# Kernel optimization log

Hardware: AMD Instinct MI355X
Metric: run time of the kernel (lower is better)

The kernel has to match this reference:

```python
import jax, jax.numpy as jnp
import numpy as np

N = 100000      # nodes
E = 6400000     # edges (avg degree 64)
S = 8           # FSM states
X = 2 ** S      # neighborhood 'characters' (256)
ITERS = 20      # NeuralFSM.iterations


def setup_inputs() -> dict:
    key = jax.random.key(0)
    k1, k2, k3 = jax.random.split(key, 3)
    # one-hot initial node states [N, S]
    state_idx = jax.random.randint(k1, (N,), 0, S)
    s0 = jax.nn.one_hot(state_idx, S, dtype=jnp.float32)
    # edge list [2, E]
    edge_index = jax.random.randint(k2, (2, E), 0, N, dtype=jnp.int32)
    # FSM transition tensor T[char, state, :] is one-hot over next state -> [X, S, S]
    next_state = jax.random.randint(k3, (X, S), 0, S)
    T = jax.nn.one_hot(next_state, S, dtype=jnp.float32)
    return {"s0": s0, "edge_index": edge_index, "T": T}


def reference(s0, edge_index, T):
    n_nodes, n_states = s0.shape
    src, dst = edge_index[0], edge_index[1]
    powers = (2 ** jnp.arange(n_states)).astype(jnp.int32)  # base-2 encoding of thresholded aggr

    def step(s, _):
        # message = x_j gathered from source nodes, scatter-added at destinations
        msg_sum = jax.ops.segment_sum(s[src], dst, num_segments=n_nodes)  # [N, S]
        # threshold (> 0.5) then clamp to {0,1}
        aggr = (msg_sum > 0.5).astype(jnp.int32)                          # [N, S]
        # multiple-hot -> index into 2^S characters (one-hot folded into a gather)
        idx = aggr @ powers                                               # [N]
        # einsum('x,s,xst->t') with one-hot char == gather T[idx] then contract state
        new_s = jnp.einsum('ns,nst->nt', s, T[idx])                       # [N, S]
        return new_s, None

    s_final, _ = jax.lax.scan(step, s0, None, length=ITERS)
    return s_final
```

## Files before the change

### kernel.cpp

```cpp
#include <hip/hip_runtime.h>
#include <hip/hip_bf16.h>
#include <stdint.h>


#define NN 100000
#define EE 6400000
#define NCHARS 2048
#define ITERS 20

#define NBKT 250
#define NPB 400
#define WPS 12500
#define X4N 3125
#define CEDGE 12800
#define NCHUNK 500
#define CAPB 27648
#define HCAP 13824

#define MEG_TOP     2080
#define CUR_OFF     3328
#define BAR_WORDS   4096

typedef uint32_t u32x4 __attribute__((ext_vector_type(4)));

__device__ inline void mega_barrier(uint32_t* bar, int line, uint32_t epoch) {
    __syncthreads();
    if (threadIdx.x == 0) {
        uint32_t old = atomicAdd(&bar[1664 + line * 16], 1u);
        if (old + 1u == 10u * epoch) {
            uint32_t told = atomicAdd(&bar[MEG_TOP], 1u);
            if (told + 1u == 25u * epoch) {
                for (int r = 0; r < 25; ++r)
                    atomicExch(&bar[2112 + r * 16], epoch);
            }
        }
        while (__hip_atomic_load(&bar[2112 + line * 16], __ATOMIC_RELAXED,
                                 __HIP_MEMORY_SCOPE_AGENT) < epoch)
            __builtin_amdgcn_s_sleep(16);
    }
    __syncthreads();
}

__global__ void __launch_bounds__(512) build_kernel(const int* __restrict__ src,
                                                    const int* __restrict__ dst,
                                                    const float* __restrict__ s0,
                                                    const float* __restrict__ T,
                                                    uint32_t* __restrict__ gPk0,
                                                    uint8_t* __restrict__ nextT,
                                                    uint32_t* __restrict__ csr,
                                                    uint32_t* __restrict__ bar) {
    __shared__ uint32_t stage[CEDGE];
    __shared__ uint32_t cw[8][256];
    __shared__ uint32_t scanb[512];
    __shared__ uint32_t loc[NBKT + 1];
    __shared__ uint32_t segoff[NBKT];
    __shared__ uint8_t  lut[CEDGE];
    int t = threadIdx.x, w = t >> 6;
    int c = blockIdx.x;
    int e0 = c * CEDGE;
    const int4* ps4 = (const int4*)(src + e0);
    const int4* pd4 = (const int4*)(dst + e0);
    uint32_t* cursorG = bar + CUR_OFF;

    if (t < 25) loc[t] = 0;
    __syncthreads();
    if (t < 200) {
        const float* row = s0 + ((size_t)c * 200 + t) * 8;
        int s = 0;
        #pragma unroll
        for (int q = 1; q < 8; ++q) if (row[q] > 0.5f) s = q;
        atomicOr(&loc[t >> 3], (uint32_t)s << ((t & 7) << 2));
    }
    __syncthreads();
    if (t < 25) gPk0[c * 25 + t] = loc[t];
    if (c < 4) {
        const float* row = T + (c * 512 + t) * 8;
        int s = 0;
        #pragma unroll
        for (int q = 1; q < 8; ++q) if (row[q] > 0.5f) s = q;
        nextT[c * 512 + t] = (uint8_t)s;
    }
    __syncthreads();

    for (int i = t; i < 8 * 256; i += 512) ((uint32_t*)cw)[i] = 0;
    __syncthreads();
    for (int i = t; i < CEDGE / 4; i += 512) {
        int4 d = pd4[i];
        atomicAdd(&cw[w][d.x / NPB], 1u);
        atomicAdd(&cw[w][d.y / NPB], 1u);
        atomicAdd(&cw[w][d.z / NPB], 1u);
        atomicAdd(&cw[w][d.w / NPB], 1u);
    }
    __syncthreads();
    uint32_t tot = 0;
    if (t < NBKT) {
        #pragma unroll
        for (int w2 = 0; w2 < 8; ++w2) tot += cw[w2][t];
    }
    scanb[t] = tot;
    __syncthreads();
    for (int off = 1; off < 512; off <<= 1) {
        uint32_t x = (t >= off) ? scanb[t - off] : 0u;
        __syncthreads();
        scanb[t] += x;
        __syncthreads();
    }
    if (t < NBKT) {
        uint32_t excl = scanb[t] - tot;
        loc[t] = excl;
        uint32_t myStart = atomicAdd(&cursorG[t], tot);
        segoff[t] = (uint32_t)t * CAPB + myStart - excl;
        uint32_t acc = excl;
        #pragma unroll
        for (int w2 = 0; w2 < 8; ++w2) {
            uint32_t cv = cw[w2][t];
            cw[w2][t] = acc;
            acc += cv;
        }
    }
    if (t == 0) loc[NBKT] = CEDGE;
    __syncthreads();
    for (int b = t; b < NBKT; b += 512) {
        uint32_t lo = loc[b], hi = loc[b + 1];
        for (uint32_t i = lo; i < hi; ++i) lut[i] = (uint8_t)b;
    }
    for (int i = t; i < CEDGE / 4; i += 512) {
        int4 d = pd4[i];
        int4 s = ps4[i];
        int bb; uint32_t dl, pos;
        bb = d.x / NPB; dl = (uint32_t)(d.x - bb * NPB);
        pos = atomicAdd(&cw[w][bb], 1u); stage[pos] = ((uint32_t)s.x << 9) | dl;
        bb = d.y / NPB; dl = (uint32_t)(d.y - bb * NPB);
        pos = atomicAdd(&cw[w][bb], 1u); stage[pos] = ((uint32_t)s.y << 9) | dl;
        bb = d.z / NPB; dl = (uint32_t)(d.z - bb * NPB);
        pos = atomicAdd(&cw[w][bb], 1u); stage[pos] = ((uint32_t)s.z << 9) | dl;
        bb = d.w / NPB; dl = (uint32_t)(d.w - bb * NPB);
        pos = atomicAdd(&cw[w][bb], 1u); stage[pos] = ((uint32_t)s.w << 9) | dl;
    }
    __syncthreads();
    for (int i = t; i < CEDGE; i += 512) {
        csr[segoff[lut[i]] + (uint32_t)i] = stage[i];
    }
}

__global__ void __launch_bounds__(512) p4_sortsrc(uint32_t* __restrict__ csr,
                                                  const uint32_t* __restrict__ cntG) {
    __shared__ uint32_t st[HCAP];
    __shared__ uint32_t binh[512];
    int t = threadIdx.x;
    int j = blockIdx.x;
    int b = j >> 1, h = j & 1;
    uint32_t n  = cntG[b];
    uint32_t n1 = (n + 1) >> 1;
    uint32_t r0 = (uint32_t)b * CAPB + (h ? n1 : 0);
    uint32_t cnt = h ? n - n1 : n1;
    if (cnt > HCAP) return;
    for (uint32_t i = t; i < cnt; i += 512) st[i] = csr[r0 + i];
    binh[t] = 0;
    __syncthreads();
    for (uint32_t i = t; i < cnt; i += 512) atomicAdd(&binh[st[i] >> 17], 1u);
    __syncthreads();
    uint32_t v = binh[t];
    __syncthreads();
    for (int off = 1; off < 512; off <<= 1) {
        uint32_t x = (t >= off) ? binh[t - off] : 0u;
        __syncthreads();
        binh[t] += x;
        __syncthreads();
    }
    uint32_t excl = binh[t] - v;
    __syncthreads();
    binh[t] = excl;
    __syncthreads();
    for (uint32_t i = t; i < cnt; i += 512) {
        uint32_t w = st[i];
        uint32_t pos = atomicAdd(&binh[w >> 17], 1u);
        csr[r0 + pos] = w;
    }
}

__global__ void __launch_bounds__(1024) mega_kernel(const uint32_t* __restrict__ csr,
                                                    uint32_t* __restrict__ gPkA,
                                                    uint32_t* __restrict__ gPkB,
                                                    const uint8_t* __restrict__ nextT,
                                                    float* __restrict__ out,
                                                    uint32_t* __restrict__ bar) {
    __shared__ uint32_t sPk[WPS];
    __shared__ uint32_t mask[NPB];
    __shared__ uint32_t packOwn[NPB / 8];
    __shared__ uint8_t  nT[NCHARS];
    __shared__ uint8_t  sown[NPB];
    int t = threadIdx.x;
    int b = blockIdx.x;
    uint32_t base = (uint32_t)b * CAPB;
    uint32_t end  = base + bar[CUR_OFF + b];

    if (t < 512) ((uint32_t*)nT)[t] = ((const uint32_t*)nextT)[t];
    const int line = b % 25;

    for (int p = 0; p < ITERS; ++p) {
        const uint32_t* curG = (p & 1) ? gPkB : gPkA;
        uint32_t*       nxtG = (p & 1) ? gPkA : gPkB;
        {
            const u32x4* g4 = (const u32x4*)curG;
            int i0 = t, i1 = t + 1024, i2 = t + 2048;
            int i3 = t + 3072; if (i3 > X4N - 1) i3 = X4N - 1;
            const u32x4 *p0 = g4 + i0, *p1 = g4 + i1, *p2 = g4 + i2, *p3 = g4 + i3;
            u32x4 a0, a1, a2, a3;
            asm volatile(
                "global_load_dwordx4 %0, %4, off sc1\n\t"
                "global_load_dwordx4 %1, %5, off sc1\n\t"
                "global_load_dwordx4 %2, %6, off sc1\n\t"
                "global_load_dwordx4 %3, %7, off sc1\n\t"
                "s_waitcnt vmcnt(0)"
                : "=&v"(a0), "=&v"(a1), "=&v"(a2), "=&v"(a3)
                : "v"(p0), "v"(p1), "v"(p2), "v"(p3)
                : "memory");
            u32x4* s4 = (u32x4*)sPk;
            s4[i0] = a0; s4[i1] = a1; s4[i2] = a2; s4[i3] = a3;
        }
        if (t < NPB) mask[t] = 0;
        if (t < NPB / 8) packOwn[t] = 0;
        __syncthreads();

        uint32_t e = base + t;
        for (; e + 3072 < end; e += 4096) {
            uint32_t w0 = csr[e], w1 = csr[e + 1024], w2 = csr[e + 2048], w3 = csr[e + 3072];
            uint32_t s0_ = w0 >> 9, s1_ = w1 >> 9, s2_ = w2 >> 9, s3_ = w3 >> 9;
            uint32_t n0 = (sPk[s0_ >> 3] >> ((s0_ & 7) << 2)) & 7u;
            uint32_t n1 = (sPk[s1_ >> 3] >> ((s1_ & 7) << 2)) & 7u;
            uint32_t n2 = (sPk[s2_ >> 3] >> ((s2_ & 7) << 2)) & 7u;
            uint32_t n3 = (sPk[s3_ >> 3] >> ((s3_ & 7) << 2)) & 7u;
            atomicOr(&mask[w0 & 511u], 1u << n0);
            atomicOr(&mask[w1 & 511u], 1u << n1);
            atomicOr(&mask[w2 & 511u], 1u << n2);
            atomicOr(&mask[w3 & 511u], 1u << n3);
        }
        for (; e < end; e += 1024) {
            uint32_t wv = csr[e];
            uint32_t s_ = wv >> 9;
            uint32_t nb = (sPk[s_ >> 3] >> ((s_ & 7) << 2)) & 7u;
            atomicOr(&mask[wv & 511u], 1u << nb);
        }
        __syncthreads();

        if (t < NPB) {
            int node = b * NPB + t;
            uint32_t sOwn = (sPk[node >> 3] >> ((node & 7) << 2)) & 7u;
            uint8_t ns = nT[(mask[t] << 3) + sOwn];
            sown[t] = ns;
            atomicOr(&packOwn[t >> 3], (uint32_t)ns << ((t & 7) << 2));
        }
        __syncthreads();
        if (p < ITERS - 1) {
            if (t < NPB / 8)
                __hip_atomic_store(&nxtG[(NPB / 8) * b + t], packOwn[t],
                                   __ATOMIC_RELAXED, __HIP_MEMORY_SCOPE_AGENT);
            mega_barrier(bar, line, (uint32_t)(p + 1));
        }
    }
    __syncthreads();
    for (int f = t; f < NPB * 8; f += 1024) {
        int node = f >> 3;
        out[(size_t)b * (NPB * 8) + f] = ((f & 7) == (int)sown[node]) ? 1.f : 0.f;
    }
}

__global__ void fb_decode(const float* __restrict__ s0, const float* __restrict__ T,
                          uint8_t* __restrict__ state, uint8_t* __restrict__ nextT,
                          uint32_t* __restrict__ mask) {
    int i = blockIdx.x * blockDim.x + threadIdx.x;
    if (i < NCHARS) {
        const float* row = T + i * 8;
        int t = 0;
        #pragma unroll
        for (int k = 1; k < 8; ++k) if (row[k] > 0.5f) t = k;
        nextT[i] = (uint8_t)t;
    }
    if (i < NN) {
        const float* row = s0 + i * 8;
        int s = 0;
        #pragma unroll
        for (int k = 1; k < 8; ++k) if (row[k] > 0.5f) s = k;
        state[i] = (uint8_t)s;
        mask[i] = 0u;
    }
}
__global__ void fb_edge(const int* __restrict__ src, const int* __restrict__ dst,
                        const uint8_t* __restrict__ state, uint32_t* __restrict__ mask) {
    int i = blockIdx.x * blockDim.x + threadIdx.x;
    int stride = gridDim.x * blockDim.x;
    for (int e = i; e < EE; e += stride) atomicOr(&mask[dst[e]], 1u << state[src[e]]);
}
__global__ void fb_update(uint8_t* __restrict__ state, uint32_t* __restrict__ mask,
                          const uint8_t* __restrict__ nextT) {
    int i = blockIdx.x * blockDim.x + threadIdx.x;
    if (i < NN) {
        uint32_t m = mask[i];
        state[i] = nextT[(m << 3) + state[i]];
        mask[i] = 0u;
    }
}
__global__ void fb_output(const uint8_t* __restrict__ state, float* __restrict__ out) {
    int i = blockIdx.x * blockDim.x + threadIdx.x;
    if (i < NN) {
        int s = state[i];
        float4 lo = make_float4(s == 0 ? 1.f : 0.f, s == 1 ? 1.f : 0.f,
                                s == 2 ? 1.f : 0.f, s == 3 ? 1.f : 0.f);
        float4 hi = make_float4(s == 4 ? 1.f : 0.f, s == 5 ? 1.f : 0.f,
                                s == 6 ? 1.f : 0.f, s == 7 ? 1.f : 0.f);
        float4* o = (float4*)(out + (size_t)i * 8);
        o[0] = lo;
        o[1] = hi;
    }
}

extern "C" void kernel_launch(void* const* d_in, const int* in_sizes, int n_in,
                              void* d_out, int out_size, void* d_ws, size_t ws_size,
                              hipStream_t stream) {
    const float* s0  = (const float*)d_in[0];
    const int*   ei  = (const int*)d_in[1];
    const float* T   = (const float*)d_in[2];
    float*       out = (float*)d_out;
    const int* src = ei;
    const int* dst = ei + EE;

    uint8_t* basep = (uint8_t*)d_ws;
    size_t off = 0;
    auto alloc = [&](size_t sz) -> void* {
        void* p = basep + off;
        off += (sz + 255) & ~(size_t)255;
        return p;
    };
    uint32_t* csr   = (uint32_t*)alloc(sizeof(uint32_t) * (size_t)NBKT * CAPB);
    uint8_t*  nextT = (uint8_t*)alloc(NCHARS);
    uint32_t* gPkA  = (uint32_t*)alloc(sizeof(uint32_t) * WPS);
    uint32_t* gPkB  = (uint32_t*)alloc(sizeof(uint32_t) * WPS);
    uint32_t* bar   = (uint32_t*)alloc(sizeof(uint32_t) * BAR_WORDS);
    bool have_ws = (off <= ws_size);

    if (have_ws) {
        hipMemsetAsync(bar, 0, sizeof(uint32_t) * BAR_WORDS, stream);
        build_kernel<<<NCHUNK, 512, 0, stream>>>(src, dst, s0, T, gPkA, nextT, csr, bar);
        p4_sortsrc<<<NBKT * 2, 512, 0, stream>>>(csr, bar + CUR_OFF);
        mega_kernel<<<NBKT, 1024, 0, stream>>>(csr, gPkA, gPkB, nextT, out, bar);
    } else {
        uint32_t* mask = (uint32_t*)d_ws;
        uint8_t*  nT   = (uint8_t*)d_ws + 400128;
        uint8_t*  st   = (uint8_t*)d_ws + 402432;
        fb_decode<<<391, 256, 0, stream>>>(s0, T, st, nT, mask);
        for (int it = 0; it < ITERS; ++it) {
            fb_edge<<<2048, 256, 0, stream>>>(src, dst, st, mask);
            fb_update<<<391, 256, 0, stream>>>(st, mask, nT);
        }
        fb_output<<<391, 256, 0, stream>>>(st, out);
    }
}
```

Measured before the change: 273.3 us.

## Pre-encode CSR edge words as byte offsets, vectorize edge loads, coalesce sort writes

Edge words are now stored with the source's word byte offset, nibble shift and destination byte offset already in place. This lets the per-iteration edge loop address the shared packed-state array and mask array with fewer shifts and masks. The mega kernel now reads the CSR as 128-bit vectors, eight edges per thread per step, with scalar tail loops for leftover edges. The source-sort pass scatters into an LDS buffer and then writes back contiguously, so global stores are coalesced. The barrier spin sleep is also shortened. The costs are extra LDS in the sort kernel and more spinning pressure on the barrier flags.

```diff
diff --git a/kernel.cpp b/kernel.cpp
--- a/kernel.cpp
+++ b/kernel.cpp
@@ -36,7 +36,7 @@
         }
         while (__hip_atomic_load(&bar[2112 + line * 16], __ATOMIC_RELAXED,
                                  __HIP_MEMORY_SCOPE_AGENT) < epoch)
-            __builtin_amdgcn_s_sleep(16);
+            __builtin_amdgcn_s_sleep(1);
     }
     __syncthreads();
 }
@@ -129,13 +129,17 @@
         int4 s = ps4[i];
         int bb; uint32_t dl, pos;
         bb = d.x / NPB; dl = (uint32_t)(d.x - bb * NPB);
-        pos = atomicAdd(&cw[w][bb], 1u); stage[pos] = ((uint32_t)s.x << 9) | dl;
+        pos = atomicAdd(&cw[w][bb], 1u);
+        stage[pos] = ((uint32_t)(s.x >> 3) << 18) | ((uint32_t)(s.x & 7) << 13) | (dl << 2);
         bb = d.y / NPB; dl = (uint32_t)(d.y - bb * NPB);
-        pos = atomicAdd(&cw[w][bb], 1u); stage[pos] = ((uint32_t)s.y << 9) | dl;
+        pos = atomicAdd(&cw[w][bb], 1u);
+        stage[pos] = ((uint32_t)(s.y >> 3) << 18) | ((uint32_t)(s.y & 7) << 13) | (dl << 2);
         bb = d.z / NPB; dl = (uint32_t)(d.z - bb * NPB);
-        pos = atomicAdd(&cw[w][bb], 1u); stage[pos] = ((uint32_t)s.z << 9) | dl;
+        pos = atomicAdd(&cw[w][bb], 1u);
+        stage[pos] = ((uint32_t)(s.z >> 3) << 18) | ((uint32_t)(s.z & 7) << 13) | (dl << 2);
         bb = d.w / NPB; dl = (uint32_t)(d.w - bb * NPB);
-        pos = atomicAdd(&cw[w][bb], 1u); stage[pos] = ((uint32_t)s.w << 9) | dl;
+        pos = atomicAdd(&cw[w][bb], 1u);
+        stage[pos] = ((uint32_t)(s.w >> 3) << 18) | ((uint32_t)(s.w & 7) << 13) | (dl << 2);
     }
     __syncthreads();
     for (int i = t; i < CEDGE; i += 512) {
@@ -146,6 +150,7 @@
 __global__ void __launch_bounds__(512) p4_sortsrc(uint32_t* __restrict__ csr,
                                                   const uint32_t* __restrict__ cntG) {
     __shared__ uint32_t st[HCAP];
+    __shared__ uint32_t ob[HCAP];
     __shared__ uint32_t binh[512];
     int t = threadIdx.x;
     int j = blockIdx.x;
@@ -158,7 +163,7 @@
     for (uint32_t i = t; i < cnt; i += 512) st[i] = csr[r0 + i];
     binh[t] = 0;
     __syncthreads();
-    for (uint32_t i = t; i < cnt; i += 512) atomicAdd(&binh[st[i] >> 17], 1u);
+    for (uint32_t i = t; i < cnt; i += 512) atomicAdd(&binh[st[i] >> 23], 1u);
     __syncthreads();
     uint32_t v = binh[t];
     __syncthreads();
@@ -174,9 +179,11 @@
     __syncthreads();
     for (uint32_t i = t; i < cnt; i += 512) {
         uint32_t w = st[i];
-        uint32_t pos = atomicAdd(&binh[w >> 17], 1u);
-        csr[r0 + pos] = w;
-    }
+        uint32_t pos = atomicAdd(&binh[w >> 23], 1u);
+        ob[pos] = w;
+    }
+    __syncthreads();
+    for (uint32_t i = t; i < cnt; i += 512) csr[r0 + i] = ob[i];
 }
 
 __global__ void __launch_bounds__(1024) mega_kernel(const uint32_t* __restrict__ csr,
@@ -223,24 +230,24 @@
         if (t < NPB / 8) packOwn[t] = 0;
         __syncthreads();
 
-        uint32_t e = base + t;
-        for (; e + 3072 < end; e += 4096) {
-            uint32_t w0 = csr[e], w1 = csr[e + 1024], w2 = csr[e + 2048], w3 = csr[e + 3072];
-            uint32_t s0_ = w0 >> 9, s1_ = w1 >> 9, s2_ = w2 >> 9, s3_ = w3 >> 9;
-            uint32_t n0 = (sPk[s0_ >> 3] >> ((s0_ & 7) << 2)) & 7u;
-            uint32_t n1 = (sPk[s1_ >> 3] >> ((s1_ & 7) << 2)) & 7u;
-            uint32_t n2 = (sPk[s2_ >> 3] >> ((s2_ & 7) << 2)) & 7u;
-            uint32_t n3 = (sPk[s3_ >> 3] >> ((s3_ & 7) << 2)) & 7u;
-            atomicOr(&mask[w0 & 511u], 1u << n0);
-            atomicOr(&mask[w1 & 511u], 1u << n1);
-            atomicOr(&mask[w2 & 511u], 1u << n2);
-            atomicOr(&mask[w3 & 511u], 1u << n3);
-        }
-        for (; e < end; e += 1024) {
-            uint32_t wv = csr[e];
-            uint32_t s_ = wv >> 9;
-            uint32_t nb = (sPk[s_ >> 3] >> ((s_ & 7) << 2)) & 7u;
-            atomicOr(&mask[wv & 511u], 1u << nb);
+        auto edge1 = [&](uint32_t wv) {
+            uint32_t val = *(const uint32_t*)((const char*)sPk + (wv >> 16));
+            uint32_t nb  = (val >> ((wv >> 11) & 31u)) & 7u;
+            atomicOr((uint32_t*)((char*)mask + (wv & 0x7FCu)), 1u << nb);
+        };
+        uint32_t e = base + ((uint32_t)t << 2);
+        for (; e + 4099 < end; e += 8192) {
+            u32x4 wa = *(const u32x4*)(csr + e);
+            u32x4 wb = *(const u32x4*)(csr + e + 4096);
+            edge1(wa.x); edge1(wa.y); edge1(wa.z); edge1(wa.w);
+            edge1(wb.x); edge1(wb.y); edge1(wb.z); edge1(wb.w);
+        }
+        for (; e + 3 < end; e += 4096) {
+            u32x4 wa = *(const u32x4*)(csr + e);
+            edge1(wa.x); edge1(wa.y); edge1(wa.z); edge1(wa.w);
+        }
+        for (; e < end; ++e) {
+            edge1(csr[e]);
         }
         __syncthreads();
 
```

Result: faster. 254.0 us (-7.1%).
